# Kernel optimization log

Measured on AMD Instinct MI355X. Metric: run time of the kernel, lower is better.

## Reference

```python
import jax, jax.numpy as jnp
import numpy as np

B, S, IN, HID, NH, HD, R, WIN, TK = 2, 2048, 64, 512, 8, 64, 64, 5, 16
C1, C2, C3 = 171, 171, 170  # hidden_dim split across 3 conv branches (512 = 171+171+170)


def _conv(xc, w, b, pad):
    y = jax.lax.conv_general_dilated(xc, w, window_strides=(1,), padding=[(pad, pad)],
                                     dimension_numbers=('NCH', 'OIH', 'NCH'))
    return jax.nn.relu(y + b[None, :, None])


def setup_inputs():
    key = jax.random.key(0)
    ks = jax.random.split(key, 22)
    p = lambda k, sh: jax.random.normal(k, sh, jnp.float32) * 0.05
    return {
        'x': jax.random.normal(ks[0], (B, S, IN), jnp.float32),
        'conv1_w': p(ks[1], (C1, IN, 3)), 'conv1_b': p(ks[2], (C1,)),
        'conv2_w': p(ks[3], (C2, IN, 5)), 'conv2_b': p(ks[4], (C2,)),
        'conv3_w': p(ks[5], (C3, IN, 7)), 'conv3_b': p(ks[6], (C3,)),
        'Wq': p(ks[7], (HID, HID)), 'bq': p(ks[8], (HID,)),
        'Wk': p(ks[9], (HID, HID)), 'bk': p(ks[10], (HID,)),
        'Wv': p(ks[11], (HID, HID)), 'bv': p(ks[12], (HID,)),
        'Wkp': p(ks[13], (R, HD)), 'bkp': p(ks[14], (R,)),
        'Wvp': p(ks[15], (R, HD)), 'bvp': p(ks[16], (R,)),
        'Wo': p(ks[17], (HID, HID)), 'bo': p(ks[18], (HID,)),
        'ln_g': jnp.ones((HID,), jnp.float32), 'ln_b': jnp.zeros((HID,), jnp.float32),
    }


def reference(x, conv1_w, conv1_b, conv2_w, conv2_b, conv3_w, conv3_b,
              Wq, bq, Wk, bk, Wv, bv, Wkp, bkp, Wvp, bvp, Wo, bo, ln_g, ln_b):
    # multi-scale conv front-end
    xc = x.transpose(0, 2, 1)  # [B, IN, S]
    h = jnp.concatenate([_conv(xc, conv1_w, conv1_b, 1),
                         _conv(xc, conv2_w, conv2_b, 2),
                         _conv(xc, conv3_w, conv3_b, 3)], axis=1).transpose(0, 2, 1)  # [B,S,HID]

    def heads(W_, b_):
        return (h @ W_.T + b_).reshape(B, S, NH, HD).transpose(0, 2, 1, 3)  # [B,NH,S,HD]

    Q, K, V = heads(Wq, bq), heads(Wk, bk), heads(Wv, bv)
    Kp = K @ Wkp.T + bkp  # [B,NH,S,R]
    Vp = V @ Wvp.T + bvp

    # local sliding-window attention; -inf masking reproduces the per-t boundary slicing
    hw = WIN // 2
    idx = jnp.arange(S)[:, None] + jnp.arange(-hw, hw + 1)[None, :]
    valid = (idx >= 0) & (idx < S)
    idxc = jnp.clip(idx, 0, S - 1)
    Kw = K[:, :, idxc, :]
    Vw = V[:, :, idxc, :]
    ls = jnp.einsum('bhsd,bhswd->bhsw', Q, Kw) / jnp.sqrt(jnp.float32(HD))
    ls = jnp.where(valid[None, None], ls, -jnp.inf)
    local = jnp.einsum('bhsw,bhswd->bhsd', jax.nn.softmax(ls, axis=-1), Vw)

    # top-k low-rank global attention (HD == R required by original einsum)
    gs = jnp.einsum('bhqd,bhkd->bhqk', Q, Kp) / jnp.sqrt(jnp.float32(R))  # [B,NH,S,S]
    tv, ti = jax.lax.top_k(gs, TK)
    tw = jax.nn.softmax(tv, axis=-1)  # [B,NH,S,TK]
    bi = jnp.arange(B)[:, None, None, None]
    hi = jnp.arange(NH)[None, :, None, None]
    topV = Vp[bi, hi, ti]  # [B,NH,S,TK,R]
    sp = jnp.einsum('bhqk,bhqkr->bhqr', tw, topV)
    sp = sp @ Wvp.T + bvp  # extra value_proj applied to sparse output, as in original

    out = ((local + sp) * 0.5).transpose(0, 2, 1, 3).reshape(B, S, HID)
    out = out @ Wo.T + bo
    res = out + h
    mu = res.mean(-1, keepdims=True)
    var = ((res - mu) ** 2).mean(-1, keepdims=True)
    return (res - mu) / jnp.sqrt(var + 1e-5) * ln_g + ln_b
```

## Files before the change

### kernel.cpp

```cpp
#include <hip/hip_runtime.h>
#include <hip/hip_bf16.h>

#define BB 2
#define SS 2048
#define INC 64
#define HIDN 512
#define NHH 8
#define HDD 64
#define SP 2054

typedef __attribute__((ext_vector_type(8))) short bf16x8;
typedef __attribute__((ext_vector_type(4))) float f32x4;

__device__ __forceinline__ short f2bf(float f) {
  union { __hip_bfloat16 h; short s; } u;
  u.h = __float2bfloat16(f);
  return u.s;
}
__device__ __forceinline__ float bf2f(short s) {
  return __uint_as_float(((unsigned)(unsigned short)s) << 16);
}

__global__ __launch_bounds__(256) void prep_kernel(
    const float* __restrict__ x, const float* __restrict__ w1,
    const float* __restrict__ b1, const float* __restrict__ w2,
    const float* __restrict__ b2, const float* __restrict__ w3,
    const float* __restrict__ b3, const float* __restrict__ Wq,
    const float* __restrict__ Wk_, const float* __restrict__ Wv_,
    const float* __restrict__ bq, const float* __restrict__ bk_,
    const float* __restrict__ bv_, const float* __restrict__ Wo,
    const float* __restrict__ Wkp, const float* __restrict__ Wvp,
    const float* __restrict__ bvp, short* __restrict__ Wallbf,
    float* __restrict__ ball, short* __restrict__ Wobf,
    short* __restrict__ Wkpbf, short* __restrict__ W2bf,
    float* __restrict__ cvec, short* __restrict__ xbfp,
    short* __restrict__ Wcbf, float* __restrict__ bcat) {
  int i0 = blockIdx.x * 256 + threadIdx.x;
  int stride = gridDim.x * 256;
  for (int idx = i0; idx < 786432; idx += stride) {
    float v;
    if (idx < 262144)      v = Wq[idx];
    else if (idx < 524288) v = Wk_[idx - 262144];
    else                   v = Wv_[idx - 524288];
    Wallbf[idx] = f2bf(v);
  }
  for (int idx = i0; idx < 262144; idx += stride) Wobf[idx] = f2bf(Wo[idx]);
  for (int idx = i0; idx < BB * SP * 64; idx += stride) {
    int row = idx >> 6, ci = idx & 63;
    int b = row / SP, pr = row - b * SP;
    int sg = pr - 3;
    float v = (sg >= 0 && sg < SS) ? x[(b * SS + sg) * 64 + ci] : 0.f;
    xbfp[idx] = f2bf(v);
  }
  for (int idx = i0; idx < 512 * 448; idx += stride) {
    int c = idx / 448;
    int rem = idx - c * 448;
    int t = rem >> 6, ci = rem & 63;
    float v = 0.f;
    if (c < 171) {
      int k = t - 2;
      if (k >= 0 && k < 3) v = w1[(c * 64 + ci) * 3 + k];
    } else if (c < 342) {
      int k = t - 1;
      if (k >= 0 && k < 5) v = w2[((c - 171) * 64 + ci) * 5 + k];
    } else {
      v = w3[((c - 342) * 64 + ci) * 7 + t];
    }
    Wcbf[idx] = f2bf(v);
  }
  for (int idx = i0; idx < 4096; idx += stride) {
    Wkpbf[idx] = f2bf(Wkp[idx]);
    int j = idx >> 6, d = idx & 63;
    float s = 0.f;
#pragma unroll 8
    for (int i = 0; i < 64; i++) s += Wvp[j * 64 + i] * Wvp[i * 64 + d];
    W2bf[idx] = f2bf(s);
  }
  if (i0 < 1536) {
    float v;
    if (i0 < 512)       v = bq[i0];
    else if (i0 < 1024) v = bk_[i0 - 512];
    else                v = bv_[i0 - 1024];
    ball[i0] = v;
  }
  if (i0 < 512) {
    float v;
    if (i0 < 171)      v = b1[i0];
    else if (i0 < 342) v = b2[i0 - 171];
    else               v = b3[i0 - 342];
    bcat[i0] = v;
  }
  if (i0 < 64) {
    float s = bvp[i0];
#pragma unroll 8
    for (int i = 0; i < 64; i++) s += bvp[i] * Wvp[i0 * 64 + i];
    cvec[i0] = s;
  }
}

__global__ __launch_bounds__(256, 4) void gemm_conv(
    const short* __restrict__ xbfp, const short* __restrict__ Wcbf,
    const float* __restrict__ bcat, short* __restrict__ hbf) {
  int m0 = blockIdx.x * 128;
  int n0 = blockIdx.y * 64;
  int tid = threadIdx.x;
  int wvv = tid >> 6, lane = tid & 63;
  int quad = lane >> 4, l16 = lane & 15;
  int mw = m0 + wvv * 32;
  int r0 = mw + l16, r1 = r0 + 16;
  int b0 = r0 >> 11, s0 = r0 & 2047;
  int b1 = r1 >> 11, s1 = r1 & 2047;
  const short* ap0 = xbfp + (size_t)(b0 * SP + s0) * 64 + quad * 8;
  const short* ap1 = xbfp + (size_t)(b1 * SP + s1) * 64 + quad * 8;
  const short* bp = Wcbf + (size_t)(n0 + l16) * 448 + quad * 8;
  f32x4 acc[2][4] = {};
  bf16x8 cA0 = *(const bf16x8*)ap0;
  bf16x8 cA1 = *(const bf16x8*)ap1;
  bf16x8 cB0 = *(const bf16x8*)(bp + 0 * 16 * 448);
  bf16x8 cB1 = *(const bf16x8*)(bp + 1 * 16 * 448);
  bf16x8 cB2 = *(const bf16x8*)(bp + 2 * 16 * 448);
  bf16x8 cB3 = *(const bf16x8*)(bp + 3 * 16 * 448);
#pragma unroll 2
  for (int ks = 0; ks < 14; ks++) {
    int offn = (ks + 1 < 14 ? ks + 1 : 13) * 32;
    bf16x8 nA0 = *(const bf16x8*)(ap0 + offn);
    bf16x8 nA1 = *(const bf16x8*)(ap1 + offn);
    bf16x8 nB0 = *(const bf16x8*)(bp + 0 * 16 * 448 + offn);
    bf16x8 nB1 = *(const bf16x8*)(bp + 1 * 16 * 448 + offn);
    bf16x8 nB2 = *(const bf16x8*)(bp + 2 * 16 * 448 + offn);
    bf16x8 nB3 = *(const bf16x8*)(bp + 3 * 16 * 448 + offn);
    acc[0][0] = __builtin_amdgcn_mfma_f32_16x16x32_bf16(cA0, cB0, acc[0][0], 0, 0, 0);
    acc[1][0] = __builtin_amdgcn_mfma_f32_16x16x32_bf16(cA1, cB0, acc[1][0], 0, 0, 0);
    acc[0][1] = __builtin_amdgcn_mfma_f32_16x16x32_bf16(cA0, cB1, acc[0][1], 0, 0, 0);
    acc[1][1] = __builtin_amdgcn_mfma_f32_16x16x32_bf16(cA1, cB1, acc[1][1], 0, 0, 0);
    acc[0][2] = __builtin_amdgcn_mfma_f32_16x16x32_bf16(cA0, cB2, acc[0][2], 0, 0, 0);
    acc[1][2] = __builtin_amdgcn_mfma_f32_16x16x32_bf16(cA1, cB2, acc[1][2], 0, 0, 0);
    acc[0][3] = __builtin_amdgcn_mfma_f32_16x16x32_bf16(cA0, cB3, acc[0][3], 0, 0, 0);
    acc[1][3] = __builtin_amdgcn_mfma_f32_16x16x32_bf16(cA1, cB3, acc[1][3], 0, 0, 0);
    cA0 = nA0; cA1 = nA1;
    cB0 = nB0; cB1 = nB1; cB2 = nB2; cB3 = nB3;
  }
#pragma unroll
  for (int mt = 0; mt < 2; mt++) {
#pragma unroll
    for (int r = 0; r < 4; r++) {
      int m = mw + mt * 16 + quad * 4 + r;
#pragma unroll
      for (int t = 0; t < 4; t++) {
        int n = n0 + t * 16 + l16;
        float v = fmaxf(acc[mt][t][r] + bcat[n], 0.f);
        hbf[(size_t)m * 512 + n] = f2bf(v);
      }
    }
  }
}

__global__ __launch_bounds__(256, 4) void gemm_qkv(
    const short* __restrict__ Abf, const short* __restrict__ Wbf,
    const float* __restrict__ bias, short* __restrict__ Qh,
    short* __restrict__ Kh, short* __restrict__ Vh) {
  int m0 = blockIdx.x * 128;
  int n0 = blockIdx.y * 64;
  int tid = threadIdx.x;
  int wvv = tid >> 6, lane = tid & 63;
  int quad = lane >> 4, l16 = lane & 15;
  int mw = m0 + wvv * 32;
  const short* ap0 = Abf + (size_t)(mw + l16) * 512 + quad * 8;
  const short* ap1 = ap0 + 16 * 512;
  const short* bp = Wbf + (size_t)(n0 + l16) * 512 + quad * 8;
  f32x4 acc[2][4] = {};
  bf16x8 cA0 = *(const bf16x8*)ap0;
  bf16x8 cA1 = *(const bf16x8*)ap1;
  bf16x8 cB0 = *(const bf16x8*)(bp + 0 * 16 * 512);
  bf16x8 cB1 = *(const bf16x8*)(bp + 1 * 16 * 512);
  bf16x8 cB2 = *(const bf16x8*)(bp + 2 * 16 * 512);
  bf16x8 cB3 = *(const bf16x8*)(bp + 3 * 16 * 512);
#pragma unroll 2
  for (int ks = 0; ks < 16; ks++) {
    int offn = (ks + 1 < 16 ? ks + 1 : 15) * 32;
    bf16x8 nA0 = *(const bf16x8*)(ap0 + offn);
    bf16x8 nA1 = *(const bf16x8*)(ap1 + offn);
    bf16x8 nB0 = *(const bf16x8*)(bp + 0 * 16 * 512 + offn);
    bf16x8 nB1 = *(const bf16x8*)(bp + 1 * 16 * 512 + offn);
    bf16x8 nB2 = *(const bf16x8*)(bp + 2 * 16 * 512 + offn);
    bf16x8 nB3 = *(const bf16x8*)(bp + 3 * 16 * 512 + offn);
    acc[0][0] = __builtin_amdgcn_mfma_f32_16x16x32_bf16(cA0, cB0, acc[0][0], 0, 0, 0);
    acc[1][0] = __builtin_amdgcn_mfma_f32_16x16x32_bf16(cA1, cB0, acc[1][0], 0, 0, 0);
    acc[0][1] = __builtin_amdgcn_mfma_f32_16x16x32_bf16(cA0, cB1, acc[0][1], 0, 0, 0);
    acc[1][1] = __builtin_amdgcn_mfma_f32_16x16x32_bf16(cA1, cB1, acc[1][1], 0, 0, 0);
    acc[0][2] = __builtin_amdgcn_mfma_f32_16x16x32_bf16(cA0, cB2, acc[0][2], 0, 0, 0);
    acc[1][2] = __builtin_amdgcn_mfma_f32_16x16x32_bf16(cA1, cB2, acc[1][2], 0, 0, 0);
    acc[0][3] = __builtin_amdgcn_mfma_f32_16x16x32_bf16(cA0, cB3, acc[0][3], 0, 0, 0);
    acc[1][3] = __builtin_amdgcn_mfma_f32_16x16x32_bf16(cA1, cB3, acc[1][3], 0, 0, 0);
    cA0 = nA0; cA1 = nA1;
    cB0 = nB0; cB1 = nB1; cB2 = nB2; cB3 = nB3;
  }
  int which = n0 >> 9;
  int head = (n0 >> 6) & 7;
  short* dst = which == 0 ? Qh : (which == 1 ? Kh : Vh);
  float scale = which == 0 ? 0.125f : 1.0f;
#pragma unroll
  for (int mt = 0; mt < 2; mt++) {
#pragma unroll
    for (int r = 0; r < 4; r++) {
      int m = mw + mt * 16 + quad * 4 + r;
      int bb = m >> 11, s = m & 2047;
      size_t rowoff = ((size_t)(bb * 8 + head) * 2048 + s) * 64;
#pragma unroll
      for (int t = 0; t < 4; t++) {
        int hd = t * 16 + l16;
        float v = acc[mt][t][r] + bias[n0 + hd];
        dst[rowoff + hd] = f2bf(v * scale);
      }
    }
  }
}

__global__ __launch_bounds__(256, 4) void kpvp_local_kernel(
    const short* __restrict__ Kh, const short* __restrict__ Vh,
    const short* __restrict__ Wkpbf, const float* __restrict__ bkp,
    const short* __restrict__ W2bf, const float* __restrict__ cvec,
    short* __restrict__ Kfrag, float* __restrict__ Vpp,
    const short* __restrict__ Qh, float* __restrict__ ctxl) {
  int tid = threadIdx.x;
  __shared__ float Sloc[4][2][16][17];
  __shared__ float wloc[4][16][8];
  if (blockIdx.x < 256) {
    int m0 = blockIdx.x * 128;
    int wvv = tid >> 6, lane = tid & 63;
    int quad = lane >> 4, l16 = lane & 15;
    int mw = m0 + wvv * 32;
    {
      const short* ap0 = Kh + (size_t)(mw + l16) * 64 + quad * 8;
      const short* ap1 = ap0 + 16 * 64;
      const short* bp = Wkpbf + l16 * 64 + quad * 8;
      bf16x8 A00 = *(const bf16x8*)ap0, A01 = *(const bf16x8*)(ap0 + 32);
      bf16x8 A10 = *(const bf16x8*)ap1, A11 = *(const bf16x8*)(ap1 + 32);
      f32x4 acc[2][4] = {};
#pragma unroll
      for (int t = 0; t < 4; t++) {
        bf16x8 B0 = *(const bf16x8*)(bp + t * 16 * 64);
        bf16x8 B1 = *(const bf16x8*)(bp + t * 16 * 64 + 32);
        acc[0][t] = __builtin_amdgcn_mfma_f32_16x16x32_bf16(A00, B0, acc[0][t], 0, 0, 0);
        acc[0][t] = __builtin_amdgcn_mfma_f32_16x16x32_bf16(A01, B1, acc[0][t], 0, 0, 0);
        acc[1][t] = __builtin_amdgcn_mfma_f32_16x16x32_bf16(A10, B0, acc[1][t], 0, 0, 0);
        acc[1][t] = __builtin_amdgcn_mfma_f32_16x16x32_bf16(A11, B1, acc[1][t], 0, 0, 0);
      }
#pragma unroll
      for (int mt = 0; mt < 2; mt++)
#pragma unroll
        for (int r = 0; r < 4; r++) {
          int m = mw + mt * 16 + quad * 4 + r;
          int m15 = m & 15;
          size_t gbase = (size_t)(m >> 4) * 1024;
#pragma unroll
          for (int t = 0; t < 4; t++) {
            int n = t * 16 + l16;
            short val = f2bf(acc[mt][t][r] + bkp[n]);
            Kfrag[gbase + (size_t)(n >> 5) * 512 +
                  ((((n & 31) >> 3) * 16 + m15) << 3) + (n & 7)] = val;
          }
        }
    }
    {
      const short* ap0 = Vh + (size_t)(mw + l16) * 64 + quad * 8;
      const short* ap1 = ap0 + 16 * 64;
      const short* bp = W2bf + l16 * 64 + quad * 8;
      bf16x8 A00 = *(const bf16x8*)ap0, A01 = *(const bf16x8*)(ap0 + 32);
      bf16x8 A10 = *(const bf16x8*)ap1, A11 = *(const bf16x8*)(ap1 + 32);
      f32x4 acc[2][4] = {};
#pragma unroll
      for (int t = 0; t < 4; t++) {
        bf16x8 B0 = *(const bf16x8*)(bp + t * 16 * 64);
        bf16x8 B1 = *(const bf16x8*)(bp + t * 16 * 64 + 32);
        acc[0][t] = __builtin_amdgcn_mfma_f32_16x16x32_bf16(A00, B0, acc[0][t], 0, 0, 0);
        acc[0][t] = __builtin_amdgcn_mfma_f32_16x16x32_bf16(A01, B1, acc[0][t], 0, 0, 0);
        acc[1][t] = __builtin_amdgcn_mfma_f32_16x16x32_bf16(A10, B0, acc[1][t], 0, 0, 0);
        acc[1][t] = __builtin_amdgcn_mfma_f32_16x16x32_bf16(A11, B1, acc[1][t], 0, 0, 0);
      }
#pragma unroll
      for (int mt = 0; mt < 2; mt++)
#pragma unroll
        for (int r = 0; r < 4; r++) {
          int m = mw + mt * 16 + quad * 4 + r;
#pragma unroll
          for (int t = 0; t < 4; t++) {
            int n = t * 16 + l16;
            Vpp[(size_t)m * 64 + n] = acc[mt][t][r] + cvec[n];
          }
        }
    }
    return;
  }
  int wv = tid >> 6;
  int tile = (blockIdx.x - 256) * 4 + wv;
  int bh = tile >> 7;
  int q0 = (tile & 127) * 16;
  int lane = tid & 63;
  int quad = lane >> 4, l16 = lane & 15;

  const short* qbase = Qh + (size_t)(bh * 2048 + q0 + l16) * 64 + quad * 8;
  bf16x8 a0 = *(const bf16x8*)qbase;
  bf16x8 a1 = *(const bf16x8*)(qbase + 32);

  int k0a = min(max(q0 - 2 + l16, 0), 2047);
  int k1a = min(q0 + 6 + l16, 2047);
  const short* kb0 = Kh + (size_t)(bh * 2048 + k0a) * 64 + quad * 8;
  const short* kb1 = Kh + (size_t)(bh * 2048 + k1a) * 64 + quad * 8;
  bf16x8 B00 = *(const bf16x8*)kb0;
  bf16x8 B01 = *(const bf16x8*)(kb0 + 32);
  bf16x8 B10 = *(const bf16x8*)kb1;
  bf16x8 B11 = *(const bf16x8*)(kb1 + 32);
  f32x4 C0 = {0.f, 0.f, 0.f, 0.f};
  f32x4 C1 = {0.f, 0.f, 0.f, 0.f};
  C0 = __builtin_amdgcn_mfma_f32_16x16x32_bf16(a0, B00, C0, 0, 0, 0);
  C0 = __builtin_amdgcn_mfma_f32_16x16x32_bf16(a1, B01, C0, 0, 0, 0);
  C1 = __builtin_amdgcn_mfma_f32_16x16x32_bf16(a0, B10, C1, 0, 0, 0);
  C1 = __builtin_amdgcn_mfma_f32_16x16x32_bf16(a1, B11, C1, 0, 0, 0);
#pragma unroll
  for (int r = 0; r < 4; r++) {
    Sloc[wv][0][quad * 4 + r][l16] = C0[r];
    Sloc[wv][1][quad * 4 + r][l16] = C1[r];
  }
  __builtin_amdgcn_wave_barrier();
  if (lane < 16) {
    int q = lane;
    float sc[5];
    bool ok[5];
#pragma unroll
    for (int j = 0; j < 5; j++) {
      int offq = q + j - 2;
      int sg = q0 + offq;
      ok[j] = (sg >= 0 && sg < SS);
      int t = offq <= 13 ? 0 : 1;
      int col = t ? offq - 6 : offq + 2;
      sc[j] = ok[j] ? Sloc[wv][t][q][col] : -3.0e38f;
    }
    float m = -3.0e38f;
#pragma unroll
    for (int j = 0; j < 5; j++) m = fmaxf(m, sc[j]);
    float e[5], l = 0.f;
#pragma unroll
    for (int j = 0; j < 5; j++) {
      e[j] = ok[j] ? __expf(sc[j] - m) : 0.f;
      l += e[j];
    }
    float inv = 1.f / l;
#pragma unroll
    for (int j = 0; j < 5; j++) wloc[wv][q][j] = e[j] * inv;
  }
  __builtin_amdgcn_wave_barrier();
  {
    int q = lane >> 2, jb = (lane & 3) * 16;
    int s = q0 + q;
    float acc[16] = {};
#pragma unroll
    for (int j = 0; j < 5; j++) {
      int sg = s + j - 2;
      if (sg >= 0 && sg < SS) {
        float w = wloc[wv][q][j];
        const short* vr = Vh + (size_t)(bh * 2048 + sg) * 64 + jb;
#pragma unroll
        for (int u = 0; u < 16; u += 4) {
          short4 v4 = *(const short4*)(vr + u);
          acc[u + 0] += w * bf2f(v4.x);
          acc[u + 1] += w * bf2f(v4.y);
          acc[u + 2] += w * bf2f(v4.z);
          acc[u + 3] += w * bf2f(v4.w);
        }
      }
    }
    float* orow = ctxl + (size_t)(bh * 2048 + s) * 64 + jb;
#pragma unroll
    for (int u = 0; u < 16; u += 4)
      *(float4*)(orow + u) =
          make_float4(acc[u], acc[u + 1], acc[u + 2], acc[u + 3]);
  }
}

__global__ __launch_bounds__(256, 4) void global_attn(
    const short* __restrict__ Qh, const short* __restrict__ Kfrag,
    const float* __restrict__ Vpp, const float* __restrict__ ctxl,
    short* __restrict__ ctxcb) {
  int tid = threadIdx.x;
  int wv = tid >> 6;
  int lane = tid & 63;
  int quad = lane >> 4, l16 = lane & 15;
  int tb = wv >> 1;
  int half = wv & 1;
  int p = blockIdx.x;
  int bh = (p & 7) * 2 + ((p >> 3) & 1);
  int seg = p >> 4;
  int tile = seg * 2 + tb;
  int q0 = tile * 16;

  __shared__ unsigned swl[4][16][17];
  __shared__ float twl[2][16][17];
  __shared__ int   txl[2][16][17];

  const short* qbase = Qh + (size_t)(bh * 2048 + q0 + l16) * 64 + quad * 8;
  bf16x8 a0 = *(const bf16x8*)qbase;
  bf16x8 a1 = *(const bf16x8*)(qbase + 32);

  const short* kf =
      Kfrag + (size_t)bh * (128 * 1024) + (size_t)half * (64 * 1024) + lane * 8;

  unsigned er[4][8];
#pragma unroll
  for (int a = 0; a < 4; a++)
#pragma unroll
    for (int j = 0; j < 8; j++) er[a][j] = 0u;

  auto insert8 = [&](unsigned (&e)[8], unsigned cand) {
    unsigned n0, n1, n2, n3, n4, n5, n6, n7;
    asm("v_max_u32 %0, %1, %2" : "=v"(n0) : "v"(e[0]), "v"(cand));
    asm("v_med3_u32 %0, %1, %2, %3" : "=v"(n1) : "v"(e[0]), "v"(e[1]), "v"(cand));
    asm("v_med3_u32 %0, %1, %2, %3" : "=v"(n2) : "v"(e[1]), "v"(e[2]), "v"(cand));
    asm("v_med3_u32 %0, %1, %2, %3" : "=v"(n3) : "v"(e[2]), "v"(e[3]), "v"(cand));
    asm("v_med3_u32 %0, %1, %2, %3" : "=v"(n4) : "v"(e[3]), "v"(e[4]), "v"(cand));
    asm("v_med3_u32 %0, %1, %2, %3" : "=v"(n5) : "v"(e[4]), "v"(e[5]), "v"(cand));
    asm("v_med3_u32 %0, %1, %2, %3" : "=v"(n6) : "v"(e[5]), "v"(e[6]), "v"(cand));
    asm("v_med3_u32 %0, %1, %2, %3" : "=v"(n7) : "v"(e[6]), "v"(e[7]), "v"(cand));
    e[0] = n0; e[1] = n1; e[2] = n2; e[3] = n3;
    e[4] = n4; e[5] = n5; e[6] = n6; e[7] = n7;
  };
  auto mkcand = [&](float s, int idxr) -> unsigned {
    unsigned u = __float_as_uint(s);
    u ^= ((unsigned)((int)u >> 31)) | 0x80000000u;
    return (u & 0xFFFFF800u) | (unsigned)idxr;
  };

  int idxb = 2047 - half * 1024 - l16;
#pragma unroll 4
  for (int g = 0; g < 64; g++) {
    bf16x8 B00 = *(const bf16x8*)(kf + g * 1024);
    bf16x8 B01 = *(const bf16x8*)(kf + g * 1024 + 512);
    f32x4 C0 = {0.f, 0.f, 0.f, 0.f};
    C0 = __builtin_amdgcn_mfma_f32_16x16x32_bf16(a0, B00, C0, 0, 0, 0);
    C0 = __builtin_amdgcn_mfma_f32_16x16x32_bf16(a1, B01, C0, 0, 0, 0);
    int idxr = idxb - (g << 4);
    insert8(er[0], mkcand(C0[0], idxr));
    insert8(er[1], mkcand(C0[1], idxr));
    insert8(er[2], mkcand(C0[2], idxr));
    insert8(er[3], mkcand(C0[3], idxr));
  }

  {
    unsigned sw[4] = {0u, 0u, 0u, 0u};
#pragma unroll
    for (int t = 0; t < 16; t++) {
#pragma unroll
      for (int a = 0; a < 4; a++) {
        unsigned w = er[a][0];
#pragma unroll
        for (int mm = 1; mm <= 8; mm <<= 1) {
          unsigned o = (unsigned)__shfl_xor((int)w, mm);
          w = w > o ? w : o;
        }
        bool pop = (er[a][0] == w);
#pragma unroll
        for (int j = 0; j < 7; j++) er[a][j] = pop ? er[a][j + 1] : er[a][j];
        er[a][7] = pop ? 0u : er[a][7];
        if (l16 == t) sw[a] = w;
      }
    }
#pragma unroll
    for (int a = 0; a < 4; a++) swl[wv][quad * 4 + a][l16] = sw[a];
  }
  __syncthreads();

  if (tid < 32) {
    int tb2 = tid >> 4, q = tid & 15;
    const unsigned* A = swl[tb2 * 2][q];
    const unsigned* Bv = swl[tb2 * 2 + 1][q];
    auto decode = [&](unsigned w) -> float {
      unsigned wb = w & 0xFFFFF800u;
      unsigned uu = (w & 0x80000000u) ? (wb ^ 0x80000000u) : ~wb;
      return (w == 0u) ? -1.0e30f : __uint_as_float(uu);
    };
    unsigned h0 = A[0], h1 = Bv[0];
    float mval = decode(h0 > h1 ? h0 : h1);
    float lsum = 0.f;
    float ev[16];
    int ki[16];
#pragma unroll
    for (int i = 0; i < 16; i++) {
      unsigned wa = A[i], wb2 = Bv[15 - i];
      unsigned w = wa > wb2 ? wa : wb2;
      float sv = decode(w);
      float ex = __expf(sv - mval);
      lsum += ex;
      ev[i] = ex;
      ki[i] = 2047 - (int)(w & 0x7FFu);
    }
    float inv = 1.f / lsum;
#pragma unroll
    for (int i = 0; i < 16; i++) {
      twl[tb2][q][i] = ev[i] * inv;
      txl[tb2][q][i] = ki[i];
    }
  }
  __syncthreads();

  {
    int tb2 = tid >> 7;
    int r = tid & 127;
    int q = r >> 3, d0 = (r & 7) * 8;
    int tile2 = seg * 2 + tb2;
    int q02 = tile2 * 16;
    int b = bh >> 3, hh = bh & 7;
    const float* vball = Vpp + (size_t)bh * (2048 * 64) + d0;
    float acc[8];
#pragma unroll
    for (int u = 0; u < 8; u++) acc[u] = 0.f;
#pragma unroll 4
    for (int j = 0; j < 16; j++) {
      float w = twl[tb2][q][j];
      const float* vr = vball + (size_t)txl[tb2][q][j] * 64;
      float4 v0 = *(const float4*)vr;
      float4 v1 = *(const float4*)(vr + 4);
      acc[0] += w * v0.x; acc[1] += w * v0.y;
      acc[2] += w * v0.z; acc[3] += w * v0.w;
      acc[4] += w * v1.x; acc[5] += w * v1.y;
      acc[6] += w * v1.z; acc[7] += w * v1.w;
    }
    int s = q02 + q;
    const float* lrow = ctxl + (size_t)(bh * 2048 + s) * 64 + d0;
    short* orow = ctxcb + (size_t)(b * 2048 + s) * 512 + hh * 64 + d0;
    float4 lv0 = *(const float4*)lrow;
    float4 lv1 = *(const float4*)(lrow + 4);
    short4 o0, o1;
    o0.x = f2bf(0.5f * (lv0.x + acc[0]));
    o0.y = f2bf(0.5f * (lv0.y + acc[1]));
    o0.z = f2bf(0.5f * (lv0.z + acc[2]));
    o0.w = f2bf(0.5f * (lv0.w + acc[3]));
    o1.x = f2bf(0.5f * (lv1.x + acc[4]));
    o1.y = f2bf(0.5f * (lv1.y + acc[5]));
    o1.z = f2bf(0.5f * (lv1.z + acc[6]));
    o1.w = f2bf(0.5f * (lv1.w + acc[7]));
    *(short4*)orow = o0;
    *(short4*)(orow + 4) = o1;
  }
}

__global__ __launch_bounds__(256, 4) void gemm_wo(
    const short* __restrict__ Abf, const short* __restrict__ Wbf,
    const float* __restrict__ bo, const short* __restrict__ hbf,
    float* __restrict__ outp) {
  int m0 = blockIdx.x * 128;
  int n0 = blockIdx.y * 64;
  int tid = threadIdx.x;
  int wvv = tid >> 6, lane = tid & 63;
  int quad = lane >> 4, l16 = lane & 15;
  int mw = m0 + wvv * 32;
  const short* ap0 = Abf + (size_t)(mw + l16) * 512 + quad * 8;
  const short* ap1 = ap0 + 16 * 512;
  const short* bp = Wbf + (size_t)(n0 + l16) * 512 + quad * 8;
  f32x4 acc[2][4] = {};
  bf16x8 cA0 = *(const bf16x8*)ap0;
  bf16x8 cA1 = *(const bf16x8*)ap1;
  bf16x8 cB0 = *(const bf16x8*)(bp + 0 * 16 * 512);
  bf16x8 cB1 = *(const bf16x8*)(bp + 1 * 16 * 512);
  bf16x8 cB2 = *(const bf16x8*)(bp + 2 * 16 * 512);
  bf16x8 cB3 = *(const bf16x8*)(bp + 3 * 16 * 512);
#pragma unroll 2
  for (int ks = 0; ks < 16; ks++) {
    int offn = (ks + 1 < 16 ? ks + 1 : 15) * 32;
    bf16x8 nA0 = *(const bf16x8*)(ap0 + offn);
    bf16x8 nA1 = *(const bf16x8*)(ap1 + offn);
    bf16x8 nB0 = *(const bf16x8*)(bp + 0 * 16 * 512 + offn);
    bf16x8 nB1 = *(const bf16x8*)(bp + 1 * 16 * 512 + offn);
    bf16x8 nB2 = *(const bf16x8*)(bp + 2 * 16 * 512 + offn);
    bf16x8 nB3 = *(const bf16x8*)(bp + 3 * 16 * 512 + offn);
    acc[0][0] = __builtin_amdgcn_mfma_f32_16x16x32_bf16(cA0, cB0, acc[0][0], 0, 0, 0);
    acc[1][0] = __builtin_amdgcn_mfma_f32_16x16x32_bf16(cA1, cB0, acc[1][0], 0, 0, 0);
    acc[0][1] = __builtin_amdgcn_mfma_f32_16x16x32_bf16(cA0, cB1, acc[0][1], 0, 0, 0);
    acc[1][1] = __builtin_amdgcn_mfma_f32_16x16x32_bf16(cA1, cB1, acc[1][1], 0, 0, 0);
    acc[0][2] = __builtin_amdgcn_mfma_f32_16x16x32_bf16(cA0, cB2, acc[0][2], 0, 0, 0);
    acc[1][2] = __builtin_amdgcn_mfma_f32_16x16x32_bf16(cA1, cB2, acc[1][2], 0, 0, 0);
    acc[0][3] = __builtin_amdgcn_mfma_f32_16x16x32_bf16(cA0, cB3, acc[0][3], 0, 0, 0);
    acc[1][3] = __builtin_amdgcn_mfma_f32_16x16x32_bf16(cA1, cB3, acc[1][3], 0, 0, 0);
    cA0 = nA0; cA1 = nA1;
    cB0 = nB0; cB1 = nB1; cB2 = nB2; cB3 = nB3;
  }
#pragma unroll
  for (int mt = 0; mt < 2; mt++) {
#pragma unroll
    for (int r = 0; r < 4; r++) {
      int m = mw + mt * 16 + quad * 4 + r;
#pragma unroll
      for (int t = 0; t < 4; t++) {
        int n = n0 + t * 16 + l16;
        outp[(size_t)m * 512 + n] =
            acc[mt][t][r] + bo[n] + bf2f(hbf[(size_t)m * 512 + n]);
      }
    }
  }
}

__global__ __launch_bounds__(256) void ln_kernel(float* __restrict__ o,
                                                 const float* __restrict__ g,
                                                 const float* __restrict__ bb) {
  int row = blockIdx.x;
  int tid = threadIdx.x;
  float v0 = o[row * 512 + tid];
  float v1 = o[row * 512 + 256 + tid];
  float s = v0 + v1;
  float s2 = v0 * v0 + v1 * v1;
#pragma unroll
  for (int off = 1; off < 64; off <<= 1) {
    s += __shfl_xor(s, off);
    s2 += __shfl_xor(s2, off);
  }
  __shared__ float ps[4], ps2[4];
  int w = tid >> 6;
  if ((tid & 63) == 0) { ps[w] = s; ps2[w] = s2; }
  __syncthreads();
  float S = ps[0] + ps[1] + ps[2] + ps[3];
  float S2 = ps2[0] + ps2[1] + ps2[2] + ps2[3];
  float mu = S * (1.f / 512.f);
  float var = S2 * (1.f / 512.f) - mu * mu;
  float inv = rsqrtf(var + 1e-5f);
  o[row * 512 + tid] = (v0 - mu) * inv * g[tid] + bb[tid];
  o[row * 512 + 256 + tid] = (v1 - mu) * inv * g[tid + 256] + bb[tid + 256];
}

extern "C" void kernel_launch(void* const* d_in, const int* in_sizes, int n_in,
                              void* d_out, int out_size, void* d_ws,
                              size_t ws_size, hipStream_t stream) {
  const float* x   = (const float*)d_in[0];
  const float* w1  = (const float*)d_in[1];
  const float* b1  = (const float*)d_in[2];
  const float* w2  = (const float*)d_in[3];
  const float* b2  = (const float*)d_in[4];
  const float* w3  = (const float*)d_in[5];
  const float* b3  = (const float*)d_in[6];
  const float* Wq  = (const float*)d_in[7];
  const float* bq  = (const float*)d_in[8];
  const float* Wk  = (const float*)d_in[9];
  const float* bk  = (const float*)d_in[10];
  const float* Wv  = (const float*)d_in[11];
  const float* bv  = (const float*)d_in[12];
  const float* Wkp = (const float*)d_in[13];
  const float* bkp = (const float*)d_in[14];
  const float* Wvp = (const float*)d_in[15];
  const float* bvp = (const float*)d_in[16];
  const float* Wo  = (const float*)d_in[17];
  const float* bo  = (const float*)d_in[18];
  const float* lng = (const float*)d_in[19];
  const float* lnb = (const float*)d_in[20];

  float* p = (float*)d_ws;
  short* Wallbf = (short*)p;  p += 786432;
  float* ball   = p;          p += 2048;
  short* Wobf   = (short*)p;  p += 262144;
  short* Wkpbf  = (short*)p;  p += 4096;
  short* W2bf   = (short*)p;  p += 4096;
  float* cvec   = p;          p += 64;
  short* xbfp   = (short*)p;  p += 262912;
  short* Wcbf   = (short*)p;  p += 229376;
  float* bcat   = p;          p += 512;
  short* hbf    = (short*)p;  p += 1048576;
  short* Qh     = (short*)p;  p += 1048576;
  short* Kh     = (short*)p;  p += 1048576;
  short* Vh     = (short*)p;  p += 1048576;
  short* Kfrag  = (short*)p;  p += 1048576;
  float* Vpp    = p;          p += 2097152;
  float* ctxl   = p;          p += 2097152;
  short* ctxcb  = (short*)p;  p += 1048576;
  float* outF   = (float*)d_out;

  prep_kernel<<<512, 256, 0, stream>>>(x, w1, b1, w2, b2, w3, b3, Wq, Wk, Wv,
                                       bq, bk, bv, Wo, Wkp, Wvp, bvp, Wallbf,
                                       ball, Wobf, Wkpbf, W2bf, cvec, xbfp,
                                       Wcbf, bcat);
  {
    dim3 g(32, 8);
    gemm_conv<<<g, 256, 0, stream>>>(xbfp, Wcbf, bcat, hbf);
  }
  {
    dim3 g(32, 24);
    gemm_qkv<<<g, 256, 0, stream>>>(hbf, Wallbf, ball, Qh, Kh, Vh);
  }
  kpvp_local_kernel<<<768, 256, 0, stream>>>(Kh, Vh, Wkpbf, bkp, W2bf, cvec,
                                             Kfrag, Vpp, Qh, ctxl);
  global_attn<<<1024, 256, 0, stream>>>(Qh, Kfrag, Vpp, ctxl, ctxcb);
  {
    dim3 g(32, 8);
    gemm_wo<<<g, 256, 0, stream>>>(ctxcb, Wobf, bo, hbf, outF);
  }
  ln_kernel<<<4096, 256, 0, stream>>>(outF, lng, lnb);
}
```

Measured before the change: 230.4 us.

## Pre-swizzle bf16 weights into MFMA fragment order and vectorize prep conversions

Result: no change. 230.2 us (-0.1%).

```diff
diff --git a/kernel.cpp b/kernel.cpp
--- a/kernel.cpp
+++ b/kernel.cpp
@@ -20,6 +20,7 @@
 __device__ __forceinline__ float bf2f(short s) {
   return __uint_as_float(((unsigned)(unsigned short)s) << 16);
 }
+
 
 __global__ __launch_bounds__(256) void prep_kernel(
     const float* __restrict__ x, const float* __restrict__ w1,
@@ -37,36 +38,80 @@
     short* __restrict__ Wcbf, float* __restrict__ bcat) {
   int i0 = blockIdx.x * 256 + threadIdx.x;
   int stride = gridDim.x * 256;
-  for (int idx = i0; idx < 786432; idx += stride) {
-    float v;
-    if (idx < 262144)      v = Wq[idx];
-    else if (idx < 524288) v = Wk_[idx - 262144];
-    else                   v = Wv_[idx - 524288];
-    Wallbf[idx] = f2bf(v);
-  }
-  for (int idx = i0; idx < 262144; idx += stride) Wobf[idx] = f2bf(Wo[idx]);
-  for (int idx = i0; idx < BB * SP * 64; idx += stride) {
-    int row = idx >> 6, ci = idx & 63;
+  for (int g = i0; g < 98304; g += stride) {
+    int n = g >> 6;
+    int k = (g & 63) << 3;
+    const float* src;
+    if (n < 512)       src = Wq  + (size_t)n * 512 + k;
+    else if (n < 1024) src = Wk_ + (size_t)(n - 512) * 512 + k;
+    else               src = Wv_ + (size_t)(n - 1024) * 512 + k;
+    float4 f0 = *(const float4*)src;
+    float4 f1 = *(const float4*)(src + 4);
+    bf16x8 v;
+    v[0] = f2bf(f0.x); v[1] = f2bf(f0.y); v[2] = f2bf(f0.z); v[3] = f2bf(f0.w);
+    v[4] = f2bf(f1.x); v[5] = f2bf(f1.y); v[6] = f2bf(f1.z); v[7] = f2bf(f1.w);
+    size_t off = (size_t)(n >> 6) * 32768 + (size_t)(k >> 5) * 2048 +
+                 (size_t)((n & 63) >> 4) * 512 +
+                 ((((k & 31) >> 3) * 16 + (n & 15)) << 3);
+    *(bf16x8*)(Wallbf + off) = v;
+  }
+  for (int g = i0; g < 32768; g += stride) {
+    int n = g >> 6;
+    int k = (g & 63) << 3;
+    const float* src = Wo + (size_t)n * 512 + k;
+    float4 f0 = *(const float4*)src;
+    float4 f1 = *(const float4*)(src + 4);
+    bf16x8 v;
+    v[0] = f2bf(f0.x); v[1] = f2bf(f0.y); v[2] = f2bf(f0.z); v[3] = f2bf(f0.w);
+    v[4] = f2bf(f1.x); v[5] = f2bf(f1.y); v[6] = f2bf(f1.z); v[7] = f2bf(f1.w);
+    size_t off = (size_t)(n >> 6) * 32768 + (size_t)(k >> 5) * 2048 +
+                 (size_t)((n & 63) >> 4) * 512 +
+                 ((((k & 31) >> 3) * 16 + (n & 15)) << 3);
+    *(bf16x8*)(Wobf + off) = v;
+  }
+  for (int g = i0; g < BB * SP * 8; g += stride) {
+    int row = g >> 3, c0 = (g & 7) << 3;
     int b = row / SP, pr = row - b * SP;
     int sg = pr - 3;
-    float v = (sg >= 0 && sg < SS) ? x[(b * SS + sg) * 64 + ci] : 0.f;
-    xbfp[idx] = f2bf(v);
-  }
-  for (int idx = i0; idx < 512 * 448; idx += stride) {
-    int c = idx / 448;
-    int rem = idx - c * 448;
-    int t = rem >> 6, ci = rem & 63;
-    float v = 0.f;
-    if (c < 171) {
-      int k = t - 2;
-      if (k >= 0 && k < 3) v = w1[(c * 64 + ci) * 3 + k];
-    } else if (c < 342) {
-      int k = t - 1;
-      if (k >= 0 && k < 5) v = w2[((c - 171) * 64 + ci) * 5 + k];
+    bf16x8 v;
+    if (sg >= 0 && sg < SS) {
+      const float* src = x + ((size_t)(b * SS + sg) << 6) + c0;
+      float4 f0 = *(const float4*)src;
+      float4 f1 = *(const float4*)(src + 4);
+      v[0] = f2bf(f0.x); v[1] = f2bf(f0.y); v[2] = f2bf(f0.z); v[3] = f2bf(f0.w);
+      v[4] = f2bf(f1.x); v[5] = f2bf(f1.y); v[6] = f2bf(f1.z); v[7] = f2bf(f1.w);
     } else {
-      v = w3[((c - 342) * 64 + ci) * 7 + t];
-    }
-    Wcbf[idx] = f2bf(v);
+#pragma unroll
+      for (int e = 0; e < 8; e++) v[e] = 0;
+    }
+    *(bf16x8*)(xbfp + ((size_t)row << 3 << 3) + c0) = v;
+  }
+  for (int g = i0; g < 28672; g += stride) {
+    int c = g / 56;
+    int rem = g - c * 56;
+    int k = rem << 3;
+    int t = k >> 6;
+    int ci0 = k & 63;
+    bf16x8 v;
+#pragma unroll
+    for (int e = 0; e < 8; e++) {
+      int ci = ci0 + e;
+      float val = 0.f;
+      if (c < 171) {
+        int kk = t - 2;
+        if (kk >= 0 && kk < 3) val = w1[(c * 64 + ci) * 3 + kk];
+      } else if (c < 342) {
+        int kk = t - 1;
+        if (kk >= 0 && kk < 5) val = w2[((c - 171) * 64 + ci) * 5 + kk];
+      } else {
+        val = w3[((c - 342) * 64 + ci) * 7 + t];
+      }
+      v[e] = f2bf(val);
+    }
+    size_t off = (size_t)(c >> 6) * 28672 + (size_t)(k >> 5) * 2048 +
+                 (size_t)((c & 63) >> 4) * 512 +
+                 ((((k & 31) >> 3) * 16 + (c & 15)) << 3);
+    *(bf16x8*)(Wcbf + off) = v;
   }
   for (int idx = i0; idx < 4096; idx += stride) {
     Wkpbf[idx] = f2bf(Wkp[idx]);
@@ -112,23 +157,25 @@
   int b1 = r1 >> 11, s1 = r1 & 2047;
   const short* ap0 = xbfp + (size_t)(b0 * SP + s0) * 64 + quad * 8;
   const short* ap1 = xbfp + (size_t)(b1 * SP + s1) * 64 + quad * 8;
-  const short* bp = Wcbf + (size_t)(n0 + l16) * 448 + quad * 8;
+  const short* bp = Wcbf + (size_t)(n0 >> 6) * 28672 + lane * 8;
   f32x4 acc[2][4] = {};
   bf16x8 cA0 = *(const bf16x8*)ap0;
   bf16x8 cA1 = *(const bf16x8*)ap1;
-  bf16x8 cB0 = *(const bf16x8*)(bp + 0 * 16 * 448);
-  bf16x8 cB1 = *(const bf16x8*)(bp + 1 * 16 * 448);
-  bf16x8 cB2 = *(const bf16x8*)(bp + 2 * 16 * 448);
-  bf16x8 cB3 = *(const bf16x8*)(bp + 3 * 16 * 448);
+  bf16x8 cB0 = *(const bf16x8*)(bp + 0 * 512);
+  bf16x8 cB1 = *(const bf16x8*)(bp + 1 * 512);
+  bf16x8 cB2 = *(const bf16x8*)(bp + 2 * 512);
+  bf16x8 cB3 = *(const bf16x8*)(bp + 3 * 512);
 #pragma unroll 2
   for (int ks = 0; ks < 14; ks++) {
-    int offn = (ks + 1 < 14 ? ks + 1 : 13) * 32;
-    bf16x8 nA0 = *(const bf16x8*)(ap0 + offn);
-    bf16x8 nA1 = *(const bf16x8*)(ap1 + offn);
-    bf16x8 nB0 = *(const bf16x8*)(bp + 0 * 16 * 448 + offn);
-    bf16x8 nB1 = *(const bf16x8*)(bp + 1 * 16 * 448 + offn);
-    bf16x8 nB2 = *(const bf16x8*)(bp + 2 * 16 * 448 + offn);
-    bf16x8 nB3 = *(const bf16x8*)(bp + 3 * 16 * 448 + offn);
+    int kn = (ks + 1 < 14 ? ks + 1 : 13);
+    int offa = kn * 32;
+    int offb = kn * 2048;
+    bf16x8 nA0 = *(const bf16x8*)(ap0 + offa);
+    bf16x8 nA1 = *(const bf16x8*)(ap1 + offa);
+    bf16x8 nB0 = *(const bf16x8*)(bp + offb + 0 * 512);
+    bf16x8 nB1 = *(const bf16x8*)(bp + offb + 1 * 512);
+    bf16x8 nB2 = *(const bf16x8*)(bp + offb + 2 * 512);
+    bf16x8 nB3 = *(const bf16x8*)(bp + offb + 3 * 512);
     acc[0][0] = __builtin_amdgcn_mfma_f32_16x16x32_bf16(cA0, cB0, acc[0][0], 0, 0, 0);
     acc[1][0] = __builtin_amdgcn_mfma_f32_16x16x32_bf16(cA1, cB0, acc[1][0], 0, 0, 0);
     acc[0][1] = __builtin_amdgcn_mfma_f32_16x16x32_bf16(cA0, cB1, acc[0][1], 0, 0, 0);
@@ -167,23 +214,25 @@
   int mw = m0 + wvv * 32;
   const short* ap0 = Abf + (size_t)(mw + l16) * 512 + quad * 8;
   const short* ap1 = ap0 + 16 * 512;
-  const short* bp = Wbf + (size_t)(n0 + l16) * 512 + quad * 8;
+  const short* bp = Wbf + (size_t)(n0 >> 6) * 32768 + lane * 8;
   f32x4 acc[2][4] = {};
   bf16x8 cA0 = *(const bf16x8*)ap0;
   bf16x8 cA1 = *(const bf16x8*)ap1;
-  bf16x8 cB0 = *(const bf16x8*)(bp + 0 * 16 * 512);
-  bf16x8 cB1 = *(const bf16x8*)(bp + 1 * 16 * 512);
-  bf16x8 cB2 = *(const bf16x8*)(bp + 2 * 16 * 512);
-  bf16x8 cB3 = *(const bf16x8*)(bp + 3 * 16 * 512);
+  bf16x8 cB0 = *(const bf16x8*)(bp + 0 * 512);
+  bf16x8 cB1 = *(const bf16x8*)(bp + 1 * 512);
+  bf16x8 cB2 = *(const bf16x8*)(bp + 2 * 512);
+  bf16x8 cB3 = *(const bf16x8*)(bp + 3 * 512);
 #pragma unroll 2
   for (int ks = 0; ks < 16; ks++) {
-    int offn = (ks + 1 < 16 ? ks + 1 : 15) * 32;
-    bf16x8 nA0 = *(const bf16x8*)(ap0 + offn);
-    bf16x8 nA1 = *(const bf16x8*)(ap1 + offn);
-    bf16x8 nB0 = *(const bf16x8*)(bp + 0 * 16 * 512 + offn);
-    bf16x8 nB1 = *(const bf16x8*)(bp + 1 * 16 * 512 + offn);
-    bf16x8 nB2 = *(const bf16x8*)(bp + 2 * 16 * 512 + offn);
-    bf16x8 nB3 = *(const bf16x8*)(bp + 3 * 16 * 512 + offn);
+    int kn = (ks + 1 < 16 ? ks + 1 : 15);
+    int offa = kn * 32;
+    int offb = kn * 2048;
+    bf16x8 nA0 = *(const bf16x8*)(ap0 + offa);
+    bf16x8 nA1 = *(const bf16x8*)(ap1 + offa);
+    bf16x8 nB0 = *(const bf16x8*)(bp + offb + 0 * 512);
+    bf16x8 nB1 = *(const bf16x8*)(bp + offb + 1 * 512);
+    bf16x8 nB2 = *(const bf16x8*)(bp + offb + 2 * 512);
+    bf16x8 nB3 = *(const bf16x8*)(bp + offb + 3 * 512);
     acc[0][0] = __builtin_amdgcn_mfma_f32_16x16x32_bf16(cA0, cB0, acc[0][0], 0, 0, 0);
     acc[1][0] = __builtin_amdgcn_mfma_f32_16x16x32_bf16(cA1, cB0, acc[1][0], 0, 0, 0);
     acc[0][1] = __builtin_amdgcn_mfma_f32_16x16x32_bf16(cA0, cB1, acc[0][1], 0, 0, 0);
@@ -555,23 +604,25 @@
   int mw = m0 + wvv * 32;
   const short* ap0 = Abf + (size_t)(mw + l16) * 512 + quad * 8;
   const short* ap1 = ap0 + 16 * 512;
-  const short* bp = Wbf + (size_t)(n0 + l16) * 512 + quad * 8;
+  const short* bp = Wbf + (size_t)(n0 >> 6) * 32768 + lane * 8;
   f32x4 acc[2][4] = {};
   bf16x8 cA0 = *(const bf16x8*)ap0;
   bf16x8 cA1 = *(const bf16x8*)ap1;
-  bf16x8 cB0 = *(const bf16x8*)(bp + 0 * 16 * 512);
-  bf16x8 cB1 = *(const bf16x8*)(bp + 1 * 16 * 512);
-  bf16x8 cB2 = *(const bf16x8*)(bp + 2 * 16 * 512);
-  bf16x8 cB3 = *(const bf16x8*)(bp + 3 * 16 * 512);
+  bf16x8 cB0 = *(const bf16x8*)(bp + 0 * 512);
+  bf16x8 cB1 = *(const bf16x8*)(bp + 1 * 512);
+  bf16x8 cB2 = *(const bf16x8*)(bp + 2 * 512);
+  bf16x8 cB3 = *(const bf16x8*)(bp + 3 * 512);
 #pragma unroll 2
   for (int ks = 0; ks < 16; ks++) {
-    int offn = (ks + 1 < 16 ? ks + 1 : 15) * 32;
-    bf16x8 nA0 = *(const bf16x8*)(ap0 + offn);
-    bf16x8 nA1 = *(const bf16x8*)(ap1 + offn);
-    bf16x8 nB0 = *(const bf16x8*)(bp + 0 * 16 * 512 + offn);
-    bf16x8 nB1 = *(const bf16x8*)(bp + 1 * 16 * 512 + offn);
-    bf16x8 nB2 = *(const bf16x8*)(bp + 2 * 16 * 512 + offn);
-    bf16x8 nB3 = *(const bf16x8*)(bp + 3 * 16 * 512 + offn);
+    int kn = (ks + 1 < 16 ? ks + 1 : 15);
+    int offa = kn * 32;
+    int offb = kn * 2048;
+    bf16x8 nA0 = *(const bf16x8*)(ap0 + offa);
+    bf16x8 nA1 = *(const bf16x8*)(ap1 + offa);
+    bf16x8 nB0 = *(const bf16x8*)(bp + offb + 0 * 512);
+    bf16x8 nB1 = *(const bf16x8*)(bp + offb + 1 * 512);
+    bf16x8 nB2 = *(const bf16x8*)(bp + offb + 2 * 512);
+    bf16x8 nB3 = *(const bf16x8*)(bp + offb + 3 * 512);
     acc[0][0] = __builtin_amdgcn_mfma_f32_16x16x32_bf16(cA0, cB0, acc[0][0], 0, 0, 0);
     acc[1][0] = __builtin_amdgcn_mfma_f32_16x16x32_bf16(cA1, cB0, acc[1][0], 0, 0, 0);
     acc[0][1] = __builtin_amdgcn_mfma_f32_16x16x32_bf16(cA0, cB1, acc[0][1], 0, 0, 0);
```
